# Performance work log

Hardware: AMD Instinct MI355X
Metric: run time of the kernel (lower is better)

Reference implementation:

```python
import jax, jax.numpy as jnp
import numpy as np

B, T, N, C = 32, 16, 256, 192
S, D = 8, 192          # num_slots, slot_dim (tokens_per_slot=1 * token_dim=192)
ITERS = 3
EPS = 1e-8
SCALE = D ** -0.5


def _ln(x, g, b):
    mu = jnp.mean(x, axis=-1, keepdims=True)
    var = jnp.var(x, axis=-1, keepdims=True)
    return (x - mu) * jax.lax.rsqrt(var + 1e-5) * g + b


def setup_inputs() -> dict:
    key = jax.random.key(0)
    ks = jax.random.split(key, 20)
    def xav(k, shape):
        fan_in, fan_out = shape[-2], shape[-1]
        lim = np.sqrt(6.0 / (fan_in + fan_out))
        return jax.random.uniform(k, shape, jnp.float32, -lim, lim)
    lim_mu = np.sqrt(6.0 / (1 + D))
    return {
        "inputs": jax.random.normal(ks[0], (B, T, N, C), jnp.float32),
        "noise": jax.random.normal(ks[1], (B, S, D), jnp.float32),
        "slots_mu": jax.random.uniform(ks[2], (1, 1, D), jnp.float32, -lim_mu, lim_mu),
        "slots_log_sigma": jax.random.uniform(ks[3], (1, 1, D), jnp.float32, -lim_mu, lim_mu),
        "ln_in_g": jnp.ones((C,)), "ln_in_b": jnp.zeros((C,)),
        "Wk": xav(ks[4], (C, D)), "Wv": xav(ks[5], (C, D)), "Wq": xav(ks[6], (D, D)),
        "ln_slots_g": jnp.ones((D,)), "ln_slots_b": jnp.zeros((D,)),
        "gru_wih": xav(ks[7], (3 * D, D)),
        "gru_whh": jnp.concatenate([np.linalg.qr(np.random.RandomState(0).randn(D, D))[0].astype(np.float32) for _ in range(3)], axis=0),
        "gru_bih": jnp.zeros((3 * D,)), "gru_bhh": jnp.zeros((3 * D,)),
        "ln_ff_g": jnp.ones((D,)), "ln_ff_b": jnp.zeros((D,)),
        "mlp_w1": xav(ks[8], (D, 4 * D)), "mlp_b1": jnp.zeros((4 * D,)),
        "mlp_w2": xav(ks[9], (4 * D, D)), "mlp_b2": jnp.zeros((D,)),
        "pr_w1": xav(ks[10], (D, D)), "pr_b1": jnp.zeros((D,)),
        "pr_w2": xav(ks[11], (D, D)), "pr_b2": jnp.zeros((D,)),
    }


def reference(inputs, noise, slots_mu, slots_log_sigma, ln_in_g, ln_in_b,
              Wk, Wv, Wq, ln_slots_g, ln_slots_b,
              gru_wih, gru_whh, gru_bih, gru_bhh,
              ln_ff_g, ln_ff_b, mlp_w1, mlp_b1, mlp_w2, mlp_b2,
              pr_w1, pr_b1, pr_w2, pr_b2):
    def gru_cell(x, h):
        gx = x @ gru_wih.T + gru_bih      # [b,S,3D]
        gh = h @ gru_whh.T + gru_bhh
        xr, xz, xn = jnp.split(gx, 3, axis=-1)
        hr, hz, hn = jnp.split(gh, 3, axis=-1)
        r = jax.nn.sigmoid(xr + hr)
        z = jax.nn.sigmoid(xz + hz)
        n = jnp.tanh(xn + r * hn)
        return (1.0 - z) * n + z * h

    x = _ln(inputs, ln_in_g, ln_in_b)                 # [b,T,n,C]
    k = (x @ Wk) * SCALE                              # [b,T,n,D]
    v = x @ Wv
    slots0 = slots_mu + jnp.exp(slots_log_sigma) * noise  # [b,S,D]

    def step(slots, kv_t):
        k_t, v_t = kv_t                               # [b,n,D]
        dots = None
        for i in range(ITERS):
            slots_prev = slots
            q = _ln(slots, ln_slots_g, ln_slots_b) @ Wq        # [b,S,D]
            dots = jnp.einsum('bnd,bsd->bns', k_t, q)          # [b,n,S]
            attn = jax.nn.softmax(dots, axis=-1) + EPS         # competitive over slots
            attn = attn / jnp.sum(attn, axis=-2, keepdims=True)
            updates = jnp.einsum('bns,bnd->bsd', attn, v_t)
            slots = gru_cell(updates, slots_prev)
            if i < ITERS - 1:
                h = _ln(slots, ln_ff_g, ln_ff_b)
                slots = slots + jax.nn.relu(h @ mlp_w1 + mlp_b1) @ mlp_w2 + mlp_b2
        out_slots = slots
        out_dots = jax.nn.softmax(dots, axis=-1)
        # prior (MLP), pred_prior_from='slots'
        slots = jax.nn.relu(slots @ pr_w1 + pr_b1) @ pr_w2 + pr_b2
        return slots, (out_slots, out_dots)

    kT = jnp.swapaxes(k, 0, 1)                        # [T,b,n,D]
    vT = jnp.swapaxes(v, 0, 1)
    _, (slots_seq, dots_seq) = jax.lax.scan(step, slots0, (kT, vT))
    slots_list = jnp.swapaxes(slots_seq, 0, 1)        # [b,T,S,D]
    dots_list = jnp.swapaxes(dots_seq, 0, 1)          # [b,T,n,S]
    return slots_list, dots_list
```

## Files before the change

kernel.cpp:

```cpp
#include <hip/hip_runtime.h>

typedef __bf16 bf16x8 __attribute__((ext_vector_type(8)));
typedef float  f32x4  __attribute__((ext_vector_type(4)));

#define ATTN_EPS 1e-8f
#define K_SCALE  0.07216878364870322f

struct __align__(16) Smem {
  float slots[8 * 192];
  __bf16 slots_bf[16 * 192];
  __bf16 ln_bf[16 * 192];
  __bf16 q_bf[16 * 192];
  __bf16 upd_bf[16 * 192];
  __bf16 attnT[16 * 256];
  __bf16 a_bf[16 * 768];
  float gx[8 * 577];
  float gh[8 * 577];
  float colsum[8];
  float Lsg[192], Lsb[192], Lfg[192], Lfb[192];
  float Bih[576], Bhh[576], B1s[768], B2s[192], Pb1s[192], Pb2s[192];
};

__device__ __forceinline__ void st_swz(__bf16* buf, int strideB, int row, int col, float v) {
  *(__bf16*)((char*)buf + row * strideB + ((col * 2) ^ ((row & 7) << 4))) = (__bf16)v;
}

__device__ __forceinline__ f32x4 zero4() { f32x4 z = {0.f, 0.f, 0.f, 0.f}; return z; }

__device__ __forceinline__ float sigm(float x) {
  return __builtin_amdgcn_rcpf(1.f + __expf(-x));
}
__device__ __forceinline__ float tanhfast(float x) {
  float a = fminf(12.f, fmaxf(-12.f, x));
  float e = __expf(2.f * a);
  return (e - 1.f) * __builtin_amdgcn_rcpf(e + 1.f);
}

template <int K>
__device__ __forceinline__ f32x4 mmcore(f32x4 acc, const __bf16* a_lds, int astrideB,
                                        const __bf16* __restrict__ Bg, int ldb,
                                        int col0, int kofs, int lane) {
  int arow = lane & 15, kgr = lane >> 4;
  const char* ab = (const char*)a_lds + arow * astrideB;
  int aswz = (arow & 7) << 4;
  const __bf16* bp = Bg + (col0 + arow) * ldb + kofs + kgr * 8;
#pragma unroll
  for (int ki = 0; ki < K; ++ki) {
    bf16x8 a = *(const bf16x8*)(ab + ((kofs * 2 + ki * 64 + kgr * 16) ^ aswz));
    bf16x8 b = *(const bf16x8*)(bp + ki * 32);
    acc = __builtin_amdgcn_mfma_f32_16x16x32_bf16(a, b, acc, 0, 0, 0);
  }
  return acc;
}

__device__ __forceinline__ void ln_row(Smem& sm, int s, int lane,
                                       const float* g, const float* bta, __bf16* dst) {
  float v0 = sm.slots[s * 192 + lane], v1 = sm.slots[s * 192 + 64 + lane], v2 = sm.slots[s * 192 + 128 + lane];
  float sum = v0 + v1 + v2, sq = v0 * v0 + v1 * v1 + v2 * v2;
#pragma unroll
  for (int m = 1; m < 64; m <<= 1) { sum += __shfl_xor(sum, m, 64); sq += __shfl_xor(sq, m, 64); }
  float mu = sum * (1.f / 192.f);
  float var = sq * (1.f / 192.f) - mu * mu;
  float rs = rsqrtf(var + 1e-5f);
  st_swz(dst, 384, s, lane,       (v0 - mu) * rs * g[lane]       + bta[lane]);
  st_swz(dst, 384, s, lane + 64,  (v1 - mu) * rs * g[lane + 64]  + bta[lane + 64]);
  st_swz(dst, 384, s, lane + 128, (v2 - mu) * rs * g[lane + 128] + bta[lane + 128]);
}

__device__ __forceinline__ void job_gh(Smem& sm, const __bf16* __restrict__ W, int j, int lane) {
  f32x4 acc = mmcore<6>(zero4(), sm.slots_bf, 384, W, 192, j * 16, 0, lane);
  int kgr = lane >> 4, arow = lane & 15;
  if (kgr < 2) {
    int col = j * 16 + arow;
#pragma unroll
    for (int rr = 0; rr < 4; rr++) sm.gh[(kgr * 4 + rr) * 577 + col] = acc[rr];
  }
}

__device__ __forceinline__ void job_gx(Smem& sm, const __bf16* __restrict__ W, int j, int lane) {
  f32x4 acc = mmcore<6>(zero4(), sm.upd_bf, 384, W, 192, j * 16, 0, lane);
  int kgr = lane >> 4, arow = lane & 15;
  if (kgr < 2) {
    int col = j * 16 + arow;
#pragma unroll
    for (int rr = 0; rr < 4; rr++) {
      float sc = __builtin_amdgcn_rcpf(sm.colsum[kgr * 4 + rr]);
      sm.gx[(kgr * 4 + rr) * 577 + col] = acc[rr] * sc;
    }
  }
}

__device__ __forceinline__ void job_q(Smem& sm, const __bf16* __restrict__ W, int j, int lane) {
  f32x4 acc = mmcore<6>(zero4(), sm.ln_bf, 384, W, 192, j * 16, 0, lane);
  int kgr = lane >> 4, arow = lane & 15;
  if (kgr < 2) {
    int col = j * 16 + arow;
#pragma unroll
    for (int rr = 0; rr < 4; rr++) st_swz(sm.q_bf, 384, kgr * 4 + rr, col, acc[rr]);
  }
}

__device__ __forceinline__ void job_upd(Smem& sm, const __bf16* __restrict__ vb, int j, int lane) {
  f32x4 acc = mmcore<8>(zero4(), sm.attnT, 512, vb, 256, j * 16, 0, lane);
  int kgr = lane >> 4, arow = lane & 15;
  if (kgr < 2) {
    int col = j * 16 + arow;
#pragma unroll
    for (int rr = 0; rr < 4; rr++) st_swz(sm.upd_bf, 384, kgr * 4 + rr, col, acc[rr]);
  }
}

__device__ __forceinline__ void job_colsum(Smem& sm, const __bf16* __restrict__ onesM, int lane) {
  f32x4 acc = mmcore<8>(zero4(), sm.attnT, 512, onesM, 256, 0, 0, lane);
  int kgr = lane >> 4, arow = lane & 15;
  if (kgr < 2 && arow == 0) {
#pragma unroll
    for (int rr = 0; rr < 4; rr++) sm.colsum[kgr * 4 + rr] = acc[rr];
  }
}

__device__ __forceinline__ void job_mlp1(Smem& sm, const __bf16* __restrict__ W, int j, int lane) {
  f32x4 acc = mmcore<6>(zero4(), sm.ln_bf, 384, W, 192, j * 16, 0, lane);
  int kgr = lane >> 4, arow = lane & 15;
  if (kgr < 2) {
    int col = j * 16 + arow;
#pragma unroll
    for (int rr = 0; rr < 4; rr++)
      st_swz(sm.a_bf, 1536, kgr * 4 + rr, col, fmaxf(acc[rr] + sm.B1s[col], 0.f));
  }
}

__device__ __forceinline__ void job_mlp2(Smem& sm, const __bf16* __restrict__ W, int j, int lane) {
  f32x4 acc = zero4();
#pragma unroll
  for (int c = 0; c < 4; c++)
    acc = mmcore<6>(acc, sm.a_bf, 1536, W, 768, j * 16, c * 192, lane);
  int kgr = lane >> 4, arow = lane & 15;
  if (kgr < 2) {
    int col = j * 16 + arow;
#pragma unroll
    for (int rr = 0; rr < 4; rr++) {
      int s = kgr * 4 + rr;
      float nv = sm.slots[s * 192 + col] + acc[rr] + sm.B2s[col];
      sm.slots[s * 192 + col] = nv;
      st_swz(sm.slots_bf, 384, s, col, nv);
    }
  }
}

__device__ __forceinline__ void job_pr1(Smem& sm, const __bf16* __restrict__ W, int j, int lane) {
  f32x4 acc = mmcore<6>(zero4(), sm.slots_bf, 384, W, 192, j * 16, 0, lane);
  int kgr = lane >> 4, arow = lane & 15;
  if (kgr < 2) {
    int col = j * 16 + arow;
#pragma unroll
    for (int rr = 0; rr < 4; rr++)
      st_swz(sm.ln_bf, 384, kgr * 4 + rr, col, fmaxf(acc[rr] + sm.Pb1s[col], 0.f));
  }
}

__device__ __forceinline__ void job_pr2(Smem& sm, const __bf16* __restrict__ W, int j, int lane) {
  f32x4 acc = mmcore<6>(zero4(), sm.ln_bf, 384, W, 192, j * 16, 0, lane);
  int kgr = lane >> 4, arow = lane & 15;
  if (kgr < 2) {
    int col = j * 16 + arow;
#pragma unroll
    for (int rr = 0; rr < 4; rr++) {
      int s = kgr * 4 + rr;
      float nv = acc[rr] + sm.Pb2s[col];
      sm.slots[s * 192 + col] = nv;
      st_swz(sm.slots_bf, 384, s, col, nv);
    }
  }
}

__device__ __forceinline__ void gates(Smem& sm, int s, int lane, bool lnff) {
  float nh[3];
#pragma unroll
  for (int j = 0; j < 3; j++) {
    int d = lane + j * 64;
    float xr = sm.gx[s * 577 + d]       + sm.Bih[d];
    float xz = sm.gx[s * 577 + 192 + d] + sm.Bih[192 + d];
    float xn = sm.gx[s * 577 + 384 + d] + sm.Bih[384 + d];
    float hr = sm.gh[s * 577 + d]       + sm.Bhh[d];
    float hz = sm.gh[s * 577 + 192 + d] + sm.Bhh[192 + d];
    float hn = sm.gh[s * 577 + 384 + d] + sm.Bhh[384 + d];
    float rg = sigm(xr + hr);
    float zg = sigm(xz + hz);
    float ng = tanhfast(xn + rg * hn);
    float hv = sm.slots[s * 192 + d];
    float v = (1.f - zg) * ng + zg * hv;
    nh[j] = v;
    sm.slots[s * 192 + d] = v;
    st_swz(sm.slots_bf, 384, s, d, v);
  }
  if (lnff) {
    float sum = nh[0] + nh[1] + nh[2], sq = nh[0] * nh[0] + nh[1] * nh[1] + nh[2] * nh[2];
#pragma unroll
    for (int m = 1; m < 64; m <<= 1) { sum += __shfl_xor(sum, m, 64); sq += __shfl_xor(sq, m, 64); }
    float mu = sum * (1.f / 192.f);
    float var = sq * (1.f / 192.f) - mu * mu;
    float rs = rsqrtf(var + 1e-5f);
#pragma unroll
    for (int j = 0; j < 3; j++) {
      int d = lane + j * 64;
      st_swz(sm.ln_bf, 384, s, d, (nh[j] - mu) * rs * sm.Lfg[d] + sm.Lfb[d]);
    }
  }
}

__global__ __launch_bounds__(256) void prep_kernel(
    const float* __restrict__ Wk, const float* __restrict__ Wv, const float* __restrict__ Wq,
    const float* __restrict__ wih, const float* __restrict__ whh,
    const float* __restrict__ w1, const float* __restrict__ w2,
    const float* __restrict__ p1, const float* __restrict__ p2,
    __bf16* __restrict__ WkvP, __bf16* __restrict__ WqP,
    __bf16* __restrict__ wihB, __bf16* __restrict__ whhB,
    __bf16* __restrict__ w1P, __bf16* __restrict__ w2P,
    __bf16* __restrict__ pr1P, __bf16* __restrict__ pr2P,
    __bf16* __restrict__ onesM) {
  int i = blockIdx.x * 256 + threadIdx.x;
  if (i < 73728) {
    int col = i / 192, c = i - col * 192;
    float v = (col < 192) ? Wk[c * 192 + col] * K_SCALE : Wv[c * 192 + (col - 192)];
    WkvP[i] = (__bf16)v; return;
  }
  i -= 73728;
  if (i < 36864) { int col = i / 192, c = i - col * 192; WqP[i] = (__bf16)Wq[c * 192 + col]; return; }
  i -= 36864;
  if (i < 110592) { wihB[i] = (__bf16)wih[i]; return; }
  i -= 110592;
  if (i < 110592) { whhB[i] = (__bf16)whh[i]; return; }
  i -= 110592;
  if (i < 147456) { int o = i / 192, c = i - o * 192; w1P[i] = (__bf16)w1[c * 768 + o]; return; }
  i -= 147456;
  if (i < 147456) { int o = i / 768, c = i - o * 768; w2P[i] = (__bf16)w2[c * 192 + o]; return; }
  i -= 147456;
  if (i < 36864) { int o = i / 192, c = i - o * 192; pr1P[i] = (__bf16)p1[c * 192 + o]; return; }
  i -= 36864;
  if (i < 36864) { int o = i / 192, c = i - o * 192; pr2P[i] = (__bf16)p2[c * 192 + o]; return; }
  i -= 36864;
  if (i < 4096) onesM[i] = (__bf16)1.f;
}

__global__ __launch_bounds__(256) void p1_kernel(
    const float* __restrict__ x_in, const float* __restrict__ lng, const float* __restrict__ lnb,
    const __bf16* __restrict__ Wkv, __bf16* __restrict__ k_all, __bf16* __restrict__ v_all) {
  __shared__ __attribute__((aligned(16))) char pool[64 * 200 * 4];
  __shared__ __attribute__((aligned(16))) __bf16 xh[64 * 192];
  __shared__ float gsh[192], bsh[192];
  float* xs = (float*)pool;
  __bf16* kst = (__bf16*)pool;
  __bf16* vst = (__bf16*)(pool + 24576);

  const int tid = threadIdx.x;
  const int blk = blockIdx.x;
  const long Rbase = (long)blk * 64;
  if (tid < 192) { gsh[tid] = lng[tid]; bsh[tid] = lnb[tid]; }

  const float* gxp = x_in + Rbase * 192;
  for (int i = tid; i < 64 * 48; i += 256) {
    int row = i / 48, c4 = i - row * 48;
    float4 v = *(const float4*)(gxp + row * 192 + c4 * 4);
    float* d = xs + row * 200 + c4 * 4;
    d[0] = v.x; d[1] = v.y; d[2] = v.z; d[3] = v.w;
  }
  __syncthreads();

  const int r = tid >> 2, coff = (tid & 3) * 48;
  float xr[48];
  const float* src = xs + r * 200 + coff;
#pragma unroll
  for (int j = 0; j < 48; j++) xr[j] = src[j];
  float s = 0.f, sq = 0.f;
#pragma unroll
  for (int j = 0; j < 48; j++) { s += xr[j]; sq += xr[j] * xr[j]; }
  s += __shfl_xor(s, 1, 64);  s += __shfl_xor(s, 2, 64);
  sq += __shfl_xor(sq, 1, 64); sq += __shfl_xor(sq, 2, 64);
  float mu = s * (1.f / 192.f);
  float var = sq * (1.f / 192.f) - mu * mu;
  float rs = rsqrtf(var + 1e-5f);
  {
    char* xrow = (char*)xh + r * 384;
    int swz = (r & 7) << 4;
#pragma unroll
    for (int j = 0; j < 6; j++) {
      bf16x8 o;
#pragma unroll
      for (int e = 0; e < 8; e++) {
        int c = coff + j * 8 + e;
        o[e] = (__bf16)((xr[j * 8 + e] - mu) * rs * gsh[c] + bsh[c]);
      }
      *(bf16x8*)(xrow + (((coff + j * 8) * 2) ^ swz)) = o;
    }
  }
  __syncthreads();

  const int w = tid >> 6, lane = tid & 63;
  const int arow = lane & 15, kgr = lane >> 4;
  const int m0 = w * 16;
  const char* ab = (const char*)xh + (m0 + arow) * 384;
  const int aswz = (arow & 7) << 4;

  for (int nt = 0; nt < 12; nt++) {
    int col = nt * 16 + arow;
    const __bf16* bp = Wkv + col * 192 + kgr * 8;
    f32x4 acc = {0.f, 0.f, 0.f, 0.f};
#pragma unroll
    for (int ki = 0; ki < 6; ki++) {
      bf16x8 a = *(const bf16x8*)(ab + ((ki * 64 + kgr * 16) ^ aswz));
      bf16x8 b = *(const bf16x8*)(bp + ki * 32);
      acc = __builtin_amdgcn_mfma_f32_16x16x32_bf16(a, b, acc, 0, 0, 0);
    }
#pragma unroll
    for (int rr = 0; rr < 4; rr++) kst[(m0 + kgr * 4 + rr) * 192 + col] = (__bf16)acc[rr];
  }
  for (int nt = 0; nt < 12; nt++) {
    int dcol = nt * 16 + arow;
    const __bf16* bp = Wkv + (192 + dcol) * 192 + kgr * 8;
    f32x4 acc = {0.f, 0.f, 0.f, 0.f};
#pragma unroll
    for (int ki = 0; ki < 6; ki++) {
      bf16x8 a = *(const bf16x8*)(ab + ((ki * 64 + kgr * 16) ^ aswz));
      bf16x8 b = *(const bf16x8*)(bp + ki * 32);
      acc = __builtin_amdgcn_mfma_f32_16x16x32_bf16(a, b, acc, 0, 0, 0);
    }
    __bf16 o0 = (__bf16)acc[0], o1 = (__bf16)acc[1], o2 = (__bf16)acc[2], o3 = (__bf16)acc[3];
    __bf16* vp = &vst[dcol * 64 + m0 + kgr * 4];
    vp[0] = o0; vp[1] = o1; vp[2] = o2; vp[3] = o3;
  }
  __syncthreads();

  {
    const uint4* s4 = (const uint4*)kst;
    uint4* d4 = (uint4*)(k_all + Rbase * 192);
    for (int i = tid; i < 1536; i += 256) d4[i] = s4[i];
  }
  {
    int bt = blk >> 2;
    int n0g = (blk & 3) * 64;
    __bf16* vout = v_all + (long)bt * 49152 + n0g;
    for (int i = tid; i < 1536; i += 256) {
      int d = i >> 3, cc = i & 7;
      *(uint4*)((char*)(vout + d * 256) + cc * 16) =
          *(const uint4*)((const char*)vst + d * 128 + cc * 16);
    }
  }
}

__global__ __launch_bounds__(1024) void p2_kernel(
    const __bf16* __restrict__ k_all, const __bf16* __restrict__ v_all,
    const __bf16* __restrict__ WqP, const __bf16* __restrict__ wihB, const __bf16* __restrict__ whhB,
    const __bf16* __restrict__ w1P, const __bf16* __restrict__ w2P,
    const __bf16* __restrict__ pr1P, const __bf16* __restrict__ pr2P,
    const __bf16* __restrict__ onesM,
    const float* __restrict__ noise, const float* __restrict__ mu_p, const float* __restrict__ lsig,
    const float* __restrict__ lnsg, const float* __restrict__ lnsb,
    const float* __restrict__ lnfg, const float* __restrict__ lnfb,
    const float* __restrict__ bih, const float* __restrict__ bhh,
    const float* __restrict__ b1p, const float* __restrict__ b2p,
    const float* __restrict__ prb1, const float* __restrict__ prb2,
    float* __restrict__ out) {
  __shared__ Smem sm;
  const int tid = threadIdx.x;
  const int w = tid >> 6, lane = tid & 63;
  const int b = blockIdx.x;
  const int kgr = lane >> 4, arow = lane & 15;

  for (int i = tid; i < 192; i += 1024) {
    sm.Lsg[i] = lnsg[i]; sm.Lsb[i] = lnsb[i]; sm.Lfg[i] = lnfg[i]; sm.Lfb[i] = lnfb[i];
    sm.B2s[i] = b2p[i]; sm.Pb1s[i] = prb1[i]; sm.Pb2s[i] = prb2[i];
  }
  for (int i = tid; i < 576; i += 1024) { sm.Bih[i] = bih[i]; sm.Bhh[i] = bhh[i]; }
  for (int i = tid; i < 768; i += 1024) sm.B1s[i] = b1p[i];
  for (int i = tid; i < 16 * 192; i += 1024) {
    sm.slots_bf[i] = (__bf16)0.f; sm.ln_bf[i] = (__bf16)0.f;
    sm.q_bf[i] = (__bf16)0.f; sm.upd_bf[i] = (__bf16)0.f;
  }
  for (int i = tid; i < 16 * 256; i += 1024) sm.attnT[i] = (__bf16)0.f;
  for (int i = tid; i < 16 * 768; i += 1024) sm.a_bf[i] = (__bf16)0.f;
  __syncthreads();
  for (int i = tid; i < 1536; i += 1024) {
    int s = i / 192, d = i - s * 192;
    float v = mu_p[d] + __expf(lsig[d]) * noise[(b * 8 + s) * 192 + d];
    sm.slots[i] = v;
    st_swz(sm.slots_bf, 384, s, d, v);
  }
  __syncthreads();

  float* out_slots = out;
  float* out_dots = out + 786432;

  for (int t = 0; t < 16; ++t) {
    const __bf16* kb = k_all + (long)(b * 16 + t) * 49152;
    const __bf16* vb = v_all + (long)(b * 16 + t) * 49152;
    for (int it = 0; it < 3; ++it) {
      if (w < 8) ln_row(sm, w, lane, sm.Lsg, sm.Lsb, sm.ln_bf);
      else { job_gh(sm, whhB, (w - 8), lane); job_gh(sm, whhB, (w - 8) + 8, lane); }
      __syncthreads();
      if (w < 12) { job_q(sm, WqP, w, lane); job_gh(sm, whhB, 16 + w, lane); }
      else { job_gh(sm, whhB, 28 + (w - 12), lane); job_gh(sm, whhB, 32 + (w - 12), lane); }
      __syncthreads();
      {
        f32x4 acc = mmcore<6>(zero4(), sm.q_bf, 384, kb, 192, w * 16, 0, lane);
        float m4 = fmaxf(fmaxf(acc[0], acc[1]), fmaxf(acc[2], acc[3]));
        float m8 = fmaxf(m4, __shfl_xor(m4, 16, 64));
        float p0 = __expf(acc[0] - m8), p1 = __expf(acc[1] - m8);
        float p2v = __expf(acc[2] - m8), p3 = __expf(acc[3] - m8);
        float s4 = p0 + p1 + p2v + p3;
        float den = s4 + __shfl_xor(s4, 16, 64);
        float rden = 1.f / den;
        if (kgr < 2) {
          int n = w * 16 + arow;
          float a0 = p0 * rden, a1 = p1 * rden, a2 = p2v * rden, a3 = p3 * rden;
          if (it == 2)
            *(float4*)(out_dots + ((long)(b * 16 + t) * 256 + n) * 8 + kgr * 4) = make_float4(a0, a1, a2, a3);
          int r0 = kgr * 4;
          st_swz(sm.attnT, 512, r0 + 0, n, a0 + ATTN_EPS);
          st_swz(sm.attnT, 512, r0 + 1, n, a1 + ATTN_EPS);
          st_swz(sm.attnT, 512, r0 + 2, n, a2 + ATTN_EPS);
          st_swz(sm.attnT, 512, r0 + 3, n, a3 + ATTN_EPS);
        }
      }
      __syncthreads();
      if (w < 12) job_upd(sm, vb, w, lane);
      else if (w == 12) job_colsum(sm, onesM, lane);
      __syncthreads();
      job_gx(sm, wihB, w, lane);
      job_gx(sm, wihB, w + 16, lane);
      if (w < 4) job_gx(sm, wihB, w + 32, lane);
      __syncthreads();
      if (w < 8) gates(sm, w, lane, it < 2);
      __syncthreads();
      if (it < 2) {
        job_mlp1(sm, w1P, w, lane);
        job_mlp1(sm, w1P, w + 16, lane);
        job_mlp1(sm, w1P, w + 32, lane);
        __syncthreads();
        if (w < 12) job_mlp2(sm, w2P, w, lane);
        __syncthreads();
      }
    }
    if (w < 12) job_pr1(sm, pr1P, w, lane);
    else {
      for (int i = (w - 12) * 64 + lane; i < 384; i += 256)
        *(float4*)(out_slots + (long)(b * 16 + t) * 1536 + i * 4) = *(const float4*)(&sm.slots[i * 4]);
    }
    __syncthreads();
    if (w < 12) job_pr2(sm, pr2P, w, lane);
    __syncthreads();
  }
}

extern "C" void kernel_launch(void* const* d_in, const int* in_sizes, int n_in,
                              void* d_out, int out_size, void* d_ws, size_t ws_size,
                              hipStream_t stream) {
  const float* inputs = (const float*)d_in[0];
  const float* noise  = (const float*)d_in[1];
  const float* mu     = (const float*)d_in[2];
  const float* lsig   = (const float*)d_in[3];
  const float* ln_in_g = (const float*)d_in[4];
  const float* ln_in_b = (const float*)d_in[5];
  const float* Wk = (const float*)d_in[6];
  const float* Wv = (const float*)d_in[7];
  const float* Wq = (const float*)d_in[8];
  const float* lnsg = (const float*)d_in[9];
  const float* lnsb = (const float*)d_in[10];
  const float* wih = (const float*)d_in[11];
  const float* whh = (const float*)d_in[12];
  const float* bih = (const float*)d_in[13];
  const float* bhh = (const float*)d_in[14];
  const float* lnfg = (const float*)d_in[15];
  const float* lnfb = (const float*)d_in[16];
  const float* w1 = (const float*)d_in[17];
  const float* b1 = (const float*)d_in[18];
  const float* w2 = (const float*)d_in[19];
  const float* b2 = (const float*)d_in[20];
  const float* pw1 = (const float*)d_in[21];
  const float* pb1 = (const float*)d_in[22];
  const float* pw2 = (const float*)d_in[23];
  const float* pb2 = (const float*)d_in[24];

  char* ws = (char*)d_ws;
  __bf16* WkvP = (__bf16*)(ws + 0);
  __bf16* WqP  = (__bf16*)(ws + 147456);
  __bf16* wihB = (__bf16*)(ws + 221184);
  __bf16* whhB = (__bf16*)(ws + 442368);
  __bf16* w1P  = (__bf16*)(ws + 663552);
  __bf16* w2P  = (__bf16*)(ws + 958464);
  __bf16* pr1P = (__bf16*)(ws + 1253376);
  __bf16* pr2P = (__bf16*)(ws + 1327104);
  __bf16* k_all = (__bf16*)(ws + 1400832);
  __bf16* v_all = (__bf16*)(ws + 51732480);
  __bf16* onesM = (__bf16*)(ws + 102064128);

  prep_kernel<<<2752, 256, 0, stream>>>(Wk, Wv, Wq, wih, whh, w1, w2, pw1, pw2,
                                        WkvP, WqP, wihB, whhB, w1P, w2P, pr1P, pr2P, onesM);
  p1_kernel<<<2048, 256, 0, stream>>>(inputs, ln_in_g, ln_in_b, WkvP, k_all, v_all);
  p2_kernel<<<32, 1024, 0, stream>>>(k_all, v_all, WqP, wihB, whhB, w1P, w2P, pr1P, pr2P, onesM,
                                     noise, mu, lsig, lnsg, lnsb, lnfg, lnfb,
                                     bih, bhh, b1, b2, pb1, pb2, (float*)d_out);
}
```

Measured before the change: 2.117 ms.

## Halve recurrent kernel block to 512 threads, replace ones-matrix colsum with shuffle partials

The serial slot-attention kernel now runs 8 waves per block instead of 16, and each wave loops over more MFMA tile jobs. The Whh gate GEMM is spread across three phases. The column-sum MFMA against a ones matrix is replaced by per-wave shuffle reductions into a partial-sum array, so the ones buffer and its prep are removed. Normalization now divides the update GEMM output rather than gx. GRU activations switch to exact tanhf and division. Fewer waves mean less barrier cost but more serial MFMA work per wave in a latency-bound recurrent loop with only 32 blocks.

```diff
diff --git a/kernel.cpp b/kernel.cpp
--- a/kernel.cpp
+++ b/kernel.cpp
@@ -16,7 +16,7 @@
   __bf16 a_bf[16 * 768];
   float gx[8 * 577];
   float gh[8 * 577];
-  float colsum[8];
+  float part_cs[16 * 8];
   float Lsg[192], Lsb[192], Lfg[192], Lfb[192];
   float Bih[576], Bhh[576], B1s[768], B2s[192], Pb1s[192], Pb2s[192];
 };
@@ -27,185 +27,48 @@
 
 __device__ __forceinline__ f32x4 zero4() { f32x4 z = {0.f, 0.f, 0.f, 0.f}; return z; }
 
-__device__ __forceinline__ float sigm(float x) {
-  return __builtin_amdgcn_rcpf(1.f + __expf(-x));
-}
-__device__ __forceinline__ float tanhfast(float x) {
-  float a = fminf(12.f, fmaxf(-12.f, x));
-  float e = __expf(2.f * a);
-  return (e - 1.f) * __builtin_amdgcn_rcpf(e + 1.f);
-}
-
 template <int K>
-__device__ __forceinline__ f32x4 mmcore(f32x4 acc, const __bf16* a_lds, int astrideB,
-                                        const __bf16* __restrict__ Bg, int ldb,
-                                        int col0, int kofs, int lane) {
-  int arow = lane & 15, kgr = lane >> 4;
-  const char* ab = (const char*)a_lds + arow * astrideB;
+__device__ __forceinline__ f32x4 mmK(f32x4 acc, const char* abase, int astrideB,
+                                     const __bf16* __restrict__ bp, int lane) {
+  int arow = lane & 15;
+  const char* ab = abase + arow * astrideB;
   int aswz = (arow & 7) << 4;
-  const __bf16* bp = Bg + (col0 + arow) * ldb + kofs + kgr * 8;
+  int kb0 = (lane >> 4) * 16;
 #pragma unroll
   for (int ki = 0; ki < K; ++ki) {
-    bf16x8 a = *(const bf16x8*)(ab + ((kofs * 2 + ki * 64 + kgr * 16) ^ aswz));
+    bf16x8 a = *(const bf16x8*)(ab + ((kb0 + ki * 64) ^ aswz));
     bf16x8 b = *(const bf16x8*)(bp + ki * 32);
     acc = __builtin_amdgcn_mfma_f32_16x16x32_bf16(a, b, acc, 0, 0, 0);
   }
   return acc;
 }
 
-__device__ __forceinline__ void ln_row(Smem& sm, int s, int lane,
-                                       const float* g, const float* bta, __bf16* dst) {
-  float v0 = sm.slots[s * 192 + lane], v1 = sm.slots[s * 192 + 64 + lane], v2 = sm.slots[s * 192 + 128 + lane];
-  float sum = v0 + v1 + v2, sq = v0 * v0 + v1 * v1 + v2 * v2;
-#pragma unroll
-  for (int m = 1; m < 64; m <<= 1) { sum += __shfl_xor(sum, m, 64); sq += __shfl_xor(sq, m, 64); }
-  float mu = sum * (1.f / 192.f);
-  float var = sq * (1.f / 192.f) - mu * mu;
-  float rs = rsqrtf(var + 1e-5f);
-  st_swz(dst, 384, s, lane,       (v0 - mu) * rs * g[lane]       + bta[lane]);
-  st_swz(dst, 384, s, lane + 64,  (v1 - mu) * rs * g[lane + 64]  + bta[lane + 64]);
-  st_swz(dst, 384, s, lane + 128, (v2 - mu) * rs * g[lane + 128] + bta[lane + 128]);
-}
-
-__device__ __forceinline__ void job_gh(Smem& sm, const __bf16* __restrict__ W, int j, int lane) {
-  f32x4 acc = mmcore<6>(zero4(), sm.slots_bf, 384, W, 192, j * 16, 0, lane);
+__device__ __forceinline__ void st_f32(float* dst577, f32x4 acc, int col0, int lane) {
   int kgr = lane >> 4, arow = lane & 15;
   if (kgr < 2) {
-    int col = j * 16 + arow;
-#pragma unroll
-    for (int rr = 0; rr < 4; rr++) sm.gh[(kgr * 4 + rr) * 577 + col] = acc[rr];
-  }
-}
-
-__device__ __forceinline__ void job_gx(Smem& sm, const __bf16* __restrict__ W, int j, int lane) {
-  f32x4 acc = mmcore<6>(zero4(), sm.upd_bf, 384, W, 192, j * 16, 0, lane);
+    int c = col0 + arow;
+#pragma unroll
+    for (int rr = 0; rr < 4; rr++) dst577[(kgr * 4 + rr) * 577 + c] = acc[rr];
+  }
+}
+
+__device__ __forceinline__ void st_q_swz(__bf16* dst, f32x4 acc, int col0, int lane) {
   int kgr = lane >> 4, arow = lane & 15;
   if (kgr < 2) {
-    int col = j * 16 + arow;
-#pragma unroll
-    for (int rr = 0; rr < 4; rr++) {
-      float sc = __builtin_amdgcn_rcpf(sm.colsum[kgr * 4 + rr]);
-      sm.gx[(kgr * 4 + rr) * 577 + col] = acc[rr] * sc;
-    }
-  }
-}
-
-__device__ __forceinline__ void job_q(Smem& sm, const __bf16* __restrict__ W, int j, int lane) {
-  f32x4 acc = mmcore<6>(zero4(), sm.ln_bf, 384, W, 192, j * 16, 0, lane);
+    int c = col0 + arow;
+#pragma unroll
+    for (int rr = 0; rr < 4; rr++) st_swz(dst, 384, kgr * 4 + rr, c, acc[rr]);
+  }
+}
+
+__device__ __forceinline__ void st_relu_swz(__bf16* dst, int strideB, f32x4 acc,
+                                            int col0, const float* bias, int lane) {
   int kgr = lane >> 4, arow = lane & 15;
   if (kgr < 2) {
-    int col = j * 16 + arow;
-#pragma unroll
-    for (int rr = 0; rr < 4; rr++) st_swz(sm.q_bf, 384, kgr * 4 + rr, col, acc[rr]);
-  }
-}
-
-__device__ __forceinline__ void job_upd(Smem& sm, const __bf16* __restrict__ vb, int j, int lane) {
-  f32x4 acc = mmcore<8>(zero4(), sm.attnT, 512, vb, 256, j * 16, 0, lane);
-  int kgr = lane >> 4, arow = lane & 15;
-  if (kgr < 2) {
-    int col = j * 16 + arow;
-#pragma unroll
-    for (int rr = 0; rr < 4; rr++) st_swz(sm.upd_bf, 384, kgr * 4 + rr, col, acc[rr]);
-  }
-}
-
-__device__ __forceinline__ void job_colsum(Smem& sm, const __bf16* __restrict__ onesM, int lane) {
-  f32x4 acc = mmcore<8>(zero4(), sm.attnT, 512, onesM, 256, 0, 0, lane);
-  int kgr = lane >> 4, arow = lane & 15;
-  if (kgr < 2 && arow == 0) {
-#pragma unroll
-    for (int rr = 0; rr < 4; rr++) sm.colsum[kgr * 4 + rr] = acc[rr];
-  }
-}
-
-__device__ __forceinline__ void job_mlp1(Smem& sm, const __bf16* __restrict__ W, int j, int lane) {
-  f32x4 acc = mmcore<6>(zero4(), sm.ln_bf, 384, W, 192, j * 16, 0, lane);
-  int kgr = lane >> 4, arow = lane & 15;
-  if (kgr < 2) {
-    int col = j * 16 + arow;
+    int c = col0 + arow;
 #pragma unroll
     for (int rr = 0; rr < 4; rr++)
-      st_swz(sm.a_bf, 1536, kgr * 4 + rr, col, fmaxf(acc[rr] + sm.B1s[col], 0.f));
-  }
-}
-
-__device__ __forceinline__ void job_mlp2(Smem& sm, const __bf16* __restrict__ W, int j, int lane) {
-  f32x4 acc = zero4();
-#pragma unroll
-  for (int c = 0; c < 4; c++)
-    acc = mmcore<6>(acc, sm.a_bf, 1536, W, 768, j * 16, c * 192, lane);
-  int kgr = lane >> 4, arow = lane & 15;
-  if (kgr < 2) {
-    int col = j * 16 + arow;
-#pragma unroll
-    for (int rr = 0; rr < 4; rr++) {
-      int s = kgr * 4 + rr;
-      float nv = sm.slots[s * 192 + col] + acc[rr] + sm.B2s[col];
-      sm.slots[s * 192 + col] = nv;
-      st_swz(sm.slots_bf, 384, s, col, nv);
-    }
-  }
-}
-
-__device__ __forceinline__ void job_pr1(Smem& sm, const __bf16* __restrict__ W, int j, int lane) {
-  f32x4 acc = mmcore<6>(zero4(), sm.slots_bf, 384, W, 192, j * 16, 0, lane);
-  int kgr = lane >> 4, arow = lane & 15;
-  if (kgr < 2) {
-    int col = j * 16 + arow;
-#pragma unroll
-    for (int rr = 0; rr < 4; rr++)
-      st_swz(sm.ln_bf, 384, kgr * 4 + rr, col, fmaxf(acc[rr] + sm.Pb1s[col], 0.f));
-  }
-}
-
-__device__ __forceinline__ void job_pr2(Smem& sm, const __bf16* __restrict__ W, int j, int lane) {
-  f32x4 acc = mmcore<6>(zero4(), sm.ln_bf, 384, W, 192, j * 16, 0, lane);
-  int kgr = lane >> 4, arow = lane & 15;
-  if (kgr < 2) {
-    int col = j * 16 + arow;
-#pragma unroll
-    for (int rr = 0; rr < 4; rr++) {
-      int s = kgr * 4 + rr;
-      float nv = acc[rr] + sm.Pb2s[col];
-      sm.slots[s * 192 + col] = nv;
-      st_swz(sm.slots_bf, 384, s, col, nv);
-    }
-  }
-}
-
-__device__ __forceinline__ void gates(Smem& sm, int s, int lane, bool lnff) {
-  float nh[3];
-#pragma unroll
-  for (int j = 0; j < 3; j++) {
-    int d = lane + j * 64;
-    float xr = sm.gx[s * 577 + d]       + sm.Bih[d];
-    float xz = sm.gx[s * 577 + 192 + d] + sm.Bih[192 + d];
-    float xn = sm.gx[s * 577 + 384 + d] + sm.Bih[384 + d];
-    float hr = sm.gh[s * 577 + d]       + sm.Bhh[d];
-    float hz = sm.gh[s * 577 + 192 + d] + sm.Bhh[192 + d];
-    float hn = sm.gh[s * 577 + 384 + d] + sm.Bhh[384 + d];
-    float rg = sigm(xr + hr);
-    float zg = sigm(xz + hz);
-    float ng = tanhfast(xn + rg * hn);
-    float hv = sm.slots[s * 192 + d];
-    float v = (1.f - zg) * ng + zg * hv;
-    nh[j] = v;
-    sm.slots[s * 192 + d] = v;
-    st_swz(sm.slots_bf, 384, s, d, v);
-  }
-  if (lnff) {
-    float sum = nh[0] + nh[1] + nh[2], sq = nh[0] * nh[0] + nh[1] * nh[1] + nh[2] * nh[2];
-#pragma unroll
-    for (int m = 1; m < 64; m <<= 1) { sum += __shfl_xor(sum, m, 64); sq += __shfl_xor(sq, m, 64); }
-    float mu = sum * (1.f / 192.f);
-    float var = sq * (1.f / 192.f) - mu * mu;
-    float rs = rsqrtf(var + 1e-5f);
-#pragma unroll
-    for (int j = 0; j < 3; j++) {
-      int d = lane + j * 64;
-      st_swz(sm.ln_bf, 384, s, d, (nh[j] - mu) * rs * sm.Lfg[d] + sm.Lfb[d]);
-    }
+      st_swz(dst, strideB, kgr * 4 + rr, c, fmaxf(acc[rr] + bias[c], 0.f));
   }
 }
 
@@ -217,8 +80,7 @@
     __bf16* __restrict__ WkvP, __bf16* __restrict__ WqP,
     __bf16* __restrict__ wihB, __bf16* __restrict__ whhB,
     __bf16* __restrict__ w1P, __bf16* __restrict__ w2P,
-    __bf16* __restrict__ pr1P, __bf16* __restrict__ pr2P,
-    __bf16* __restrict__ onesM) {
+    __bf16* __restrict__ pr1P, __bf16* __restrict__ pr2P) {
   int i = blockIdx.x * 256 + threadIdx.x;
   if (i < 73728) {
     int col = i / 192, c = i - col * 192;
@@ -238,9 +100,7 @@
   i -= 147456;
   if (i < 36864) { int o = i / 192, c = i - o * 192; pr1P[i] = (__bf16)p1[c * 192 + o]; return; }
   i -= 36864;
-  if (i < 36864) { int o = i / 192, c = i - o * 192; pr2P[i] = (__bf16)p2[c * 192 + o]; return; }
-  i -= 36864;
-  if (i < 4096) onesM[i] = (__bf16)1.f;
+  { int o = i / 192, c = i - o * 192; pr2P[i] = (__bf16)p2[c * 192 + o]; }
 }
 
 __global__ __launch_bounds__(256) void p1_kernel(
@@ -299,35 +159,24 @@
   const int w = tid >> 6, lane = tid & 63;
   const int arow = lane & 15, kgr = lane >> 4;
   const int m0 = w * 16;
-  const char* ab = (const char*)xh + (m0 + arow) * 384;
-  const int aswz = (arow & 7) << 4;
-
+  const char* abase = (const char*)xh + m0 * 384;
+
+#pragma unroll 1
   for (int nt = 0; nt < 12; nt++) {
     int col = nt * 16 + arow;
     const __bf16* bp = Wkv + col * 192 + kgr * 8;
-    f32x4 acc = {0.f, 0.f, 0.f, 0.f};
-#pragma unroll
-    for (int ki = 0; ki < 6; ki++) {
-      bf16x8 a = *(const bf16x8*)(ab + ((ki * 64 + kgr * 16) ^ aswz));
-      bf16x8 b = *(const bf16x8*)(bp + ki * 32);
-      acc = __builtin_amdgcn_mfma_f32_16x16x32_bf16(a, b, acc, 0, 0, 0);
-    }
+    f32x4 acc = mmK<6>(zero4(), abase, 384, bp, lane);
 #pragma unroll
     for (int rr = 0; rr < 4; rr++) kst[(m0 + kgr * 4 + rr) * 192 + col] = (__bf16)acc[rr];
   }
+#pragma unroll 1
   for (int nt = 0; nt < 12; nt++) {
     int dcol = nt * 16 + arow;
     const __bf16* bp = Wkv + (192 + dcol) * 192 + kgr * 8;
-    f32x4 acc = {0.f, 0.f, 0.f, 0.f};
-#pragma unroll
-    for (int ki = 0; ki < 6; ki++) {
-      bf16x8 a = *(const bf16x8*)(ab + ((ki * 64 + kgr * 16) ^ aswz));
-      bf16x8 b = *(const bf16x8*)(bp + ki * 32);
-      acc = __builtin_amdgcn_mfma_f32_16x16x32_bf16(a, b, acc, 0, 0, 0);
-    }
-    __bf16 o0 = (__bf16)acc[0], o1 = (__bf16)acc[1], o2 = (__bf16)acc[2], o3 = (__bf16)acc[3];
+    f32x4 acc = mmK<6>(zero4(), abase, 384, bp, lane);
     __bf16* vp = &vst[dcol * 64 + m0 + kgr * 4];
-    vp[0] = o0; vp[1] = o1; vp[2] = o2; vp[3] = o3;
+#pragma unroll
+    for (int rr = 0; rr < 4; rr++) vp[rr] = (__bf16)acc[rr];
   }
   __syncthreads();
 
@@ -348,12 +197,12 @@
   }
 }
 
-__global__ __launch_bounds__(1024) void p2_kernel(
+__global__ __launch_bounds__(512, 1) void p2_kernel(
     const __bf16* __restrict__ k_all, const __bf16* __restrict__ v_all,
-    const __bf16* __restrict__ WqP, const __bf16* __restrict__ wihB, const __bf16* __restrict__ whhB,
+    const __bf16* __restrict__ WqP,
+    const __bf16* __restrict__ wihB, const __bf16* __restrict__ whhB,
     const __bf16* __restrict__ w1P, const __bf16* __restrict__ w2P,
     const __bf16* __restrict__ pr1P, const __bf16* __restrict__ pr2P,
-    const __bf16* __restrict__ onesM,
     const float* __restrict__ noise, const float* __restrict__ mu_p, const float* __restrict__ lsig,
     const float* __restrict__ lnsg, const float* __restrict__ lnsb,
     const float* __restrict__ lnfg, const float* __restrict__ lnfb,
@@ -367,22 +216,22 @@
   const int b = blockIdx.x;
   const int kgr = lane >> 4, arow = lane & 15;
 
-  for (int i = tid; i < 192; i += 1024) {
+  for (int i = tid; i < 192; i += 512) {
     sm.Lsg[i] = lnsg[i]; sm.Lsb[i] = lnsb[i]; sm.Lfg[i] = lnfg[i]; sm.Lfb[i] = lnfb[i];
     sm.B2s[i] = b2p[i]; sm.Pb1s[i] = prb1[i]; sm.Pb2s[i] = prb2[i];
   }
-  for (int i = tid; i < 576; i += 1024) { sm.Bih[i] = bih[i]; sm.Bhh[i] = bhh[i]; }
-  for (int i = tid; i < 768; i += 1024) sm.B1s[i] = b1p[i];
-  for (int i = tid; i < 16 * 192; i += 1024) {
+  for (int i = tid; i < 576; i += 512) { sm.Bih[i] = bih[i]; sm.Bhh[i] = bhh[i]; }
+  for (int i = tid; i < 768; i += 512) sm.B1s[i] = b1p[i];
+  for (int i = tid; i < 16 * 192; i += 512) {
     sm.slots_bf[i] = (__bf16)0.f; sm.ln_bf[i] = (__bf16)0.f;
     sm.q_bf[i] = (__bf16)0.f; sm.upd_bf[i] = (__bf16)0.f;
   }
-  for (int i = tid; i < 16 * 256; i += 1024) sm.attnT[i] = (__bf16)0.f;
-  for (int i = tid; i < 16 * 768; i += 1024) sm.a_bf[i] = (__bf16)0.f;
+  for (int i = tid; i < 16 * 256; i += 512) sm.attnT[i] = (__bf16)0.f;
+  for (int i = tid; i < 16 * 768; i += 512) sm.a_bf[i] = (__bf16)0.f;
   __syncthreads();
-  for (int i = tid; i < 1536; i += 1024) {
+  for (int i = tid; i < 1536; i += 512) {
     int s = i / 192, d = i - s * 192;
-    float v = mu_p[d] + __expf(lsig[d]) * noise[(b * 8 + s) * 192 + d];
+    float v = mu_p[d] + expf(lsig[d]) * noise[(b * 8 + s) * 192 + d];
     sm.slots[i] = v;
     st_swz(sm.slots_bf, 384, s, d, v);
   }
@@ -391,63 +240,211 @@
   float* out_slots = out;
   float* out_dots = out + 786432;
 
+#pragma unroll 1
   for (int t = 0; t < 16; ++t) {
-    const __bf16* kb = k_all + (long)(b * 16 + t) * 49152;
-    const __bf16* vb = v_all + (long)(b * 16 + t) * 49152;
+    const int bt = b * 16 + t;
+    const __bf16* kb = k_all + (long)bt * 49152;
+    const __bf16* vb = v_all + (long)bt * 49152;
+#pragma unroll 1
     for (int it = 0; it < 3; ++it) {
-      if (w < 8) ln_row(sm, w, lane, sm.Lsg, sm.Lsb, sm.ln_bf);
-      else { job_gh(sm, whhB, (w - 8), lane); job_gh(sm, whhB, (w - 8) + 8, lane); }
-      __syncthreads();
-      if (w < 12) { job_q(sm, WqP, w, lane); job_gh(sm, whhB, 16 + w, lane); }
-      else { job_gh(sm, whhB, 28 + (w - 12), lane); job_gh(sm, whhB, 32 + (w - 12), lane); }
-      __syncthreads();
       {
-        f32x4 acc = mmcore<6>(zero4(), sm.q_bf, 384, kb, 192, w * 16, 0, lane);
+        int s = w;
+        float v0 = sm.slots[s * 192 + lane], v1 = sm.slots[s * 192 + 64 + lane], v2 = sm.slots[s * 192 + 128 + lane];
+        float sum = v0 + v1 + v2, sq = v0 * v0 + v1 * v1 + v2 * v2;
+#pragma unroll
+        for (int m = 1; m < 64; m <<= 1) { sum += __shfl_xor(sum, m, 64); sq += __shfl_xor(sq, m, 64); }
+        float mu = sum * (1.f / 192.f);
+        float var = sq * (1.f / 192.f) - mu * mu;
+        float rs = rsqrtf(var + 1e-5f);
+        st_swz(sm.ln_bf, 384, s, lane,       (v0 - mu) * rs * sm.Lsg[lane]       + sm.Lsb[lane]);
+        st_swz(sm.ln_bf, 384, s, lane + 64,  (v1 - mu) * rs * sm.Lsg[lane + 64]  + sm.Lsb[lane + 64]);
+        st_swz(sm.ln_bf, 384, s, lane + 128, (v2 - mu) * rs * sm.Lsg[lane + 128] + sm.Lsb[lane + 128]);
+      }
+      __syncthreads();
+#pragma unroll 1
+      for (int jx = w; jx < 16; jx += 8) {
+        if (jx < 12) {
+          const __bf16* bp = WqP + (jx * 16 + arow) * 192 + kgr * 8;
+          f32x4 acc = mmK<6>(zero4(), (const char*)sm.ln_bf, 384, bp, lane);
+          st_q_swz(sm.q_bf, acc, jx * 16, lane);
+        } else {
+          int j2 = jx - 12;
+          const __bf16* bp = whhB + (j2 * 16 + arow) * 192 + kgr * 8;
+          f32x4 acc = mmK<6>(zero4(), (const char*)sm.slots_bf, 384, bp, lane);
+          st_f32(sm.gh, acc, j2 * 16, lane);
+        }
+      }
+      __syncthreads();
+#pragma unroll 1
+      for (int j = w; j < 16; j += 8) {
+        const __bf16* bp = kb + (j * 16 + arow) * 192 + kgr * 8;
+        f32x4 acc = mmK<6>(zero4(), (const char*)sm.q_bf, 384, bp, lane);
         float m4 = fmaxf(fmaxf(acc[0], acc[1]), fmaxf(acc[2], acc[3]));
         float m8 = fmaxf(m4, __shfl_xor(m4, 16, 64));
-        float p0 = __expf(acc[0] - m8), p1 = __expf(acc[1] - m8);
-        float p2v = __expf(acc[2] - m8), p3 = __expf(acc[3] - m8);
-        float s4 = p0 + p1 + p2v + p3;
+        float e0 = __expf(acc[0] - m8), e1 = __expf(acc[1] - m8);
+        float e2 = __expf(acc[2] - m8), e3 = __expf(acc[3] - m8);
+        float s4 = e0 + e1 + e2 + e3;
         float den = s4 + __shfl_xor(s4, 16, 64);
         float rden = 1.f / den;
         if (kgr < 2) {
-          int n = w * 16 + arow;
-          float a0 = p0 * rden, a1 = p1 * rden, a2 = p2v * rden, a3 = p3 * rden;
+          int n = j * 16 + arow;
+          float a0 = e0 * rden, a1 = e1 * rden, a2 = e2 * rden, a3 = e3 * rden;
           if (it == 2)
-            *(float4*)(out_dots + ((long)(b * 16 + t) * 256 + n) * 8 + kgr * 4) = make_float4(a0, a1, a2, a3);
+            *(float4*)(out_dots + ((long)bt * 256 + n) * 8 + kgr * 4) = make_float4(a0, a1, a2, a3);
+          __bf16 q0 = (__bf16)(a0 + ATTN_EPS), q1 = (__bf16)(a1 + ATTN_EPS);
+          __bf16 q2 = (__bf16)(a2 + ATTN_EPS), q3 = (__bf16)(a3 + ATTN_EPS);
           int r0 = kgr * 4;
-          st_swz(sm.attnT, 512, r0 + 0, n, a0 + ATTN_EPS);
-          st_swz(sm.attnT, 512, r0 + 1, n, a1 + ATTN_EPS);
-          st_swz(sm.attnT, 512, r0 + 2, n, a2 + ATTN_EPS);
-          st_swz(sm.attnT, 512, r0 + 3, n, a3 + ATTN_EPS);
-        }
-      }
-      __syncthreads();
-      if (w < 12) job_upd(sm, vb, w, lane);
-      else if (w == 12) job_colsum(sm, onesM, lane);
-      __syncthreads();
-      job_gx(sm, wihB, w, lane);
-      job_gx(sm, wihB, w + 16, lane);
-      if (w < 4) job_gx(sm, wihB, w + 32, lane);
-      __syncthreads();
-      if (w < 8) gates(sm, w, lane, it < 2);
+          char* base = (char*)sm.attnT;
+          *(__bf16*)(base + (r0 + 0) * 512 + ((n * 2) ^ (((r0 + 0) & 7) << 4))) = q0;
+          *(__bf16*)(base + (r0 + 1) * 512 + ((n * 2) ^ (((r0 + 1) & 7) << 4))) = q1;
+          *(__bf16*)(base + (r0 + 2) * 512 + ((n * 2) ^ (((r0 + 2) & 7) << 4))) = q2;
+          *(__bf16*)(base + (r0 + 3) * 512 + ((n * 2) ^ (((r0 + 3) & 7) << 4))) = q3;
+          float c0 = (float)q0, c1 = (float)q1, c2 = (float)q2, c3 = (float)q3;
+#pragma unroll
+          for (int m = 1; m < 16; m <<= 1) {
+            c0 += __shfl_xor(c0, m, 64); c1 += __shfl_xor(c1, m, 64);
+            c2 += __shfl_xor(c2, m, 64); c3 += __shfl_xor(c3, m, 64);
+          }
+          if (arow == 0) {
+            sm.part_cs[j * 8 + r0 + 0] = c0; sm.part_cs[j * 8 + r0 + 1] = c1;
+            sm.part_cs[j * 8 + r0 + 2] = c2; sm.part_cs[j * 8 + r0 + 3] = c3;
+          }
+        }
+      }
+      __syncthreads();
+      {
+        float cs[4];
+#pragma unroll
+        for (int rr = 0; rr < 4; rr++) {
+          float s = 0.f;
+#pragma unroll 1
+          for (int jj = 0; jj < 16; jj++) s += sm.part_cs[jj * 8 + ((kgr * 4 + rr) & 7)];
+          cs[rr] = s;
+        }
+#pragma unroll 1
+        for (int jx = w; jx < 40; jx += 8) {
+          if (jx < 12) {
+            const __bf16* bp = vb + (jx * 16 + arow) * 256 + kgr * 8;
+            f32x4 acc = mmK<8>(zero4(), (const char*)sm.attnT, 512, bp, lane);
+            if (kgr < 2) {
+              int col = jx * 16 + arow;
+#pragma unroll
+              for (int rr = 0; rr < 4; rr++)
+                st_swz(sm.upd_bf, 384, kgr * 4 + rr, col, acc[rr] / cs[rr]);
+            }
+          } else {
+            int j2 = jx - 8;
+            const __bf16* bp = whhB + (j2 * 16 + arow) * 192 + kgr * 8;
+            f32x4 acc = mmK<6>(zero4(), (const char*)sm.slots_bf, 384, bp, lane);
+            st_f32(sm.gh, acc, j2 * 16, lane);
+          }
+        }
+      }
+      __syncthreads();
+#pragma unroll 1
+      for (int jx = w; jx < 40; jx += 8) {
+        if (jx < 36) {
+          const __bf16* bp = wihB + (jx * 16 + arow) * 192 + kgr * 8;
+          f32x4 acc = mmK<6>(zero4(), (const char*)sm.upd_bf, 384, bp, lane);
+          st_f32(sm.gx, acc, jx * 16, lane);
+        } else {
+          int j2 = jx - 4;
+          const __bf16* bp = whhB + (j2 * 16 + arow) * 192 + kgr * 8;
+          f32x4 acc = mmK<6>(zero4(), (const char*)sm.slots_bf, 384, bp, lane);
+          st_f32(sm.gh, acc, j2 * 16, lane);
+        }
+      }
+      __syncthreads();
+      {
+        int s = w;
+        float nh[3];
+#pragma unroll
+        for (int j = 0; j < 3; j++) {
+          int d = lane + j * 64;
+          float xr = sm.gx[s * 577 + d]       + sm.Bih[d];
+          float xz = sm.gx[s * 577 + 192 + d] + sm.Bih[192 + d];
+          float xn = sm.gx[s * 577 + 384 + d] + sm.Bih[384 + d];
+          float hr = sm.gh[s * 577 + d]       + sm.Bhh[d];
+          float hz = sm.gh[s * 577 + 192 + d] + sm.Bhh[192 + d];
+          float hn = sm.gh[s * 577 + 384 + d] + sm.Bhh[384 + d];
+          float rg = 1.f / (1.f + __expf(-(xr + hr)));
+          float zg = 1.f / (1.f + __expf(-(xz + hz)));
+          float ng = tanhf(xn + rg * hn);
+          float hv = sm.slots[s * 192 + d];
+          float v = (1.f - zg) * ng + zg * hv;
+          nh[j] = v;
+          sm.slots[s * 192 + d] = v;
+          st_swz(sm.slots_bf, 384, s, d, v);
+        }
+        if (it < 2) {
+          float sum = nh[0] + nh[1] + nh[2], sq = nh[0] * nh[0] + nh[1] * nh[1] + nh[2] * nh[2];
+#pragma unroll
+          for (int m = 1; m < 64; m <<= 1) { sum += __shfl_xor(sum, m, 64); sq += __shfl_xor(sq, m, 64); }
+          float mu = sum * (1.f / 192.f);
+          float var = sq * (1.f / 192.f) - mu * mu;
+          float rs = rsqrtf(var + 1e-5f);
+#pragma unroll
+          for (int j = 0; j < 3; j++) {
+            int d = lane + j * 64;
+            st_swz(sm.ln_bf, 384, s, d, (nh[j] - mu) * rs * sm.Lfg[d] + sm.Lfb[d]);
+          }
+        }
+      }
       __syncthreads();
       if (it < 2) {
-        job_mlp1(sm, w1P, w, lane);
-        job_mlp1(sm, w1P, w + 16, lane);
-        job_mlp1(sm, w1P, w + 32, lane);
+#pragma unroll 1
+        for (int j = w; j < 48; j += 8) {
+          const __bf16* bp = w1P + (j * 16 + arow) * 192 + kgr * 8;
+          f32x4 acc = mmK<6>(zero4(), (const char*)sm.ln_bf, 384, bp, lane);
+          st_relu_swz(sm.a_bf, 1536, acc, j * 16, sm.B1s, lane);
+        }
         __syncthreads();
-        if (w < 12) job_mlp2(sm, w2P, w, lane);
+#pragma unroll 1
+        for (int j = w; j < 12; j += 8) {
+          f32x4 acc = zero4();
+#pragma unroll 1
+          for (int c = 0; c < 4; c++) {
+            const __bf16* bp = w2P + (j * 16 + arow) * 768 + c * 192 + kgr * 8;
+            acc = mmK<6>(acc, (const char*)sm.a_bf + c * 384, 1536, bp, lane);
+          }
+          if (kgr < 2) {
+            int col = j * 16 + arow;
+#pragma unroll
+            for (int rr = 0; rr < 4; rr++) {
+              int s = kgr * 4 + rr;
+              float nv = sm.slots[s * 192 + col] + acc[rr] + sm.B2s[col];
+              sm.slots[s * 192 + col] = nv;
+              st_swz(sm.slots_bf, 384, s, col, nv);
+            }
+          }
+        }
         __syncthreads();
       }
     }
-    if (w < 12) job_pr1(sm, pr1P, w, lane);
-    else {
-      for (int i = (w - 12) * 64 + lane; i < 384; i += 256)
-        *(float4*)(out_slots + (long)(b * 16 + t) * 1536 + i * 4) = *(const float4*)(&sm.slots[i * 4]);
+#pragma unroll 1
+    for (int j = w; j < 12; j += 8) {
+      const __bf16* bp = pr1P + (j * 16 + arow) * 192 + kgr * 8;
+      f32x4 acc = mmK<6>(zero4(), (const char*)sm.slots_bf, 384, bp, lane);
+      st_relu_swz(sm.ln_bf, 384, acc, j * 16, sm.Pb1s, lane);
     }
+    for (int i = tid; i < 384; i += 512)
+      *(float4*)(out_slots + (long)bt * 1536 + i * 4) = *(const float4*)(&sm.slots[i * 4]);
     __syncthreads();
-    if (w < 12) job_pr2(sm, pr2P, w, lane);
+#pragma unroll 1
+    for (int j = w; j < 12; j += 8) {
+      const __bf16* bp = pr2P + (j * 16 + arow) * 192 + kgr * 8;
+      f32x4 acc = mmK<6>(zero4(), (const char*)sm.ln_bf, 384, bp, lane);
+      if (kgr < 2) {
+        int col = j * 16 + arow;
+#pragma unroll
+        for (int rr = 0; rr < 4; rr++) {
+          int s = kgr * 4 + rr;
+          float nv = acc[rr] + sm.Pb2s[col];
+          sm.slots[s * 192 + col] = nv;
+          st_swz(sm.slots_bf, 384, s, col, nv);
+        }
+      }
+    }
     __syncthreads();
   }
 }
@@ -492,12 +489,11 @@
   __bf16* pr2P = (__bf16*)(ws + 1327104);
   __bf16* k_all = (__bf16*)(ws + 1400832);
   __bf16* v_all = (__bf16*)(ws + 51732480);
-  __bf16* onesM = (__bf16*)(ws + 102064128);
-
-  prep_kernel<<<2752, 256, 0, stream>>>(Wk, Wv, Wq, wih, whh, w1, w2, pw1, pw2,
-                                        WkvP, WqP, wihB, whhB, w1P, w2P, pr1P, pr2P, onesM);
+
+  prep_kernel<<<2736, 256, 0, stream>>>(Wk, Wv, Wq, wih, whh, w1, w2, pw1, pw2,
+                                        WkvP, WqP, wihB, whhB, w1P, w2P, pr1P, pr2P);
   p1_kernel<<<2048, 256, 0, stream>>>(inputs, ln_in_g, ln_in_b, WkvP, k_all, v_all);
-  p2_kernel<<<32, 1024, 0, stream>>>(k_all, v_all, WqP, wihB, whhB, w1P, w2P, pr1P, pr2P, onesM,
-                                     noise, mu, lsig, lnsg, lnsb, lnfg, lnfb,
-                                     bih, bhh, b1, b2, pb1, pb2, (float*)d_out);
-}
+  p2_kernel<<<32, 512, 0, stream>>>(k_all, v_all, WqP, wihB, whhB, w1P, w2P, pr1P, pr2P,
+                                    noise, mu, lsig, lnsg, lnsb, lnfg, lnfb,
+                                    bih, bhh, b1, b2, pb1, pb2, (float*)d_out);
+}
```

After: 2.086 ms. Within noise of the previous version (-1.5%).
